# Kernel optimization log

Hardware: AMD Instinct MI355X
Metric: run time of the kernel (lower is better)

Reference implementation:

```python
import jax, jax.numpy as jnp
import numpy as np

T, B, I, H, O = 1024, 512, 32, 256, 32

def setup_inputs() -> dict:
    key = jax.random.key(0)
    ks = jax.random.split(key, 8)
    s_ih = 1.0 / np.sqrt(H)
    return {
        "input_states": jax.random.normal(ks[0], (T, B, I), jnp.float32),
        "physical_predictions": jax.random.normal(ks[1], (T, B, O), jnp.float32),
        "W_ih": jax.random.uniform(ks[2], (4 * H, I), jnp.float32, -s_ih, s_ih),
        "W_hh": jax.random.uniform(ks[3], (4 * H, H), jnp.float32, -s_ih, s_ih),
        "b_ih": jax.random.uniform(ks[4], (4 * H,), jnp.float32, -s_ih, s_ih),
        "b_hh": jax.random.uniform(ks[5], (4 * H,), jnp.float32, -s_ih, s_ih),
        "W_out": jax.random.uniform(ks[6], (O, H), jnp.float32, -s_ih, s_ih),
        "b_out": jax.random.uniform(ks[7], (O,), jnp.float32, -s_ih, s_ih),
    }

def reference(input_states, physical_predictions, W_ih, W_hh, b_ih, b_hh, W_out, b_out):
    # Teacher-forced LSTM rollout (teacher_force_probability=0 -> always use input_sequence[t]),
    # use_physics_as_bias=1 -> full_pred = physical_predictions[t] + linear(h_t).
    Bsz = input_states.shape[1]
    Hd = W_hh.shape[1]
    dt = input_states.dtype

    def step(carry, xs):
        h, c = carry
        x, phys = xs                                   # [B,I], [B,O]
        gates = x @ W_ih.T + b_ih + h @ W_hh.T + b_hh  # [B,4H]
        i_g, f_g, g_g, o_g = jnp.split(gates, 4, axis=-1)
        i_g = jax.nn.sigmoid(i_g)
        f_g = jax.nn.sigmoid(f_g)
        g_g = jnp.tanh(g_g)
        o_g = jax.nn.sigmoid(o_g)
        c = f_g * c + i_g * g_g
        h = o_g * jnp.tanh(c)
        rnn_pred = h @ W_out.T + b_out                 # [B,O]
        full_pred = phys + rnn_pred
        return (h, c), (full_pred, rnn_pred)

    h0 = jnp.zeros((Bsz, Hd), dt)
    c0 = jnp.zeros((Bsz, Hd), dt)
    _, (full_preds, rnn_preds) = jax.lax.scan(step, (h0, c0), (input_states, physical_predictions))
    # torch.stack(preds, 1) -> [B, T, O]
    return jnp.transpose(full_preds, (1, 0, 2)), jnp.transpose(rnn_preds, (1, 0, 2))
```

## Files before the change

kernel.cpp:

```cpp
#include <hip/hip_runtime.h>
#include <hip/hip_bf16.h>
#include <stdint.h>

typedef unsigned short u16;
typedef unsigned long long u64;
typedef __attribute__((ext_vector_type(8))) _Float16 f16x8;
typedef __attribute__((ext_vector_type(4))) float f32x4;

#define TSTEPS 1024
#define BATCH  512
#define INDIM  32
#define HID    256
#define ODIM   32
#define NCH    66
#define KCH    9

#define WS_BC   (NCH*KCH*64*8*2)
#define WS_XBUF (WS_BC + 4096)

#define MFMA(a,b,c) __builtin_amdgcn_mfma_f32_16x16x32_f16((a),(b),(c),0,0,0)
#define AGL(p)   __hip_atomic_load((p),      __ATOMIC_RELAXED, __HIP_MEMORY_SCOPE_AGENT)
#define AGS(p,v) __hip_atomic_store((p),(v), __ATOMIC_RELAXED, __HIP_MEMORY_SCOPE_AGENT)

__device__ __forceinline__ u16 f2h(float v){ _Float16 h=(_Float16)v; return *(u16*)&h; }
__device__ __forceinline__ float sigf(float x){ return 1.0f/(1.0f+__expf(-x)); }
__device__ __forceinline__ float tanhf_(float x){
    float ax=fabsf(x); float e=__expf(-2.f*ax); float t=(1.f-e)/(1.f+e); return copysignf(t,x);
}
__device__ __forceinline__ f16x8 frag_from_u64(u64 lo, u64 hi){
    union { u64 q[2]; f16x8 v; } u; u.q[0]=lo; u.q[1]=hi; return u.v;
}
__device__ __forceinline__ f16x8 cvt8(float4 a, float4 b){
    f16x8 r;
    r[0]=(_Float16)a.x; r[1]=(_Float16)a.y; r[2]=(_Float16)a.z; r[3]=(_Float16)a.w;
    r[4]=(_Float16)b.x; r[5]=(_Float16)b.y; r[6]=(_Float16)b.z; r[7]=(_Float16)b.w;
    return r;
}

__global__ __launch_bounds__(256) void prepack_kernel(
    const float* __restrict__ W_ih, const float* __restrict__ W_hh,
    const float* __restrict__ b_ih, const float* __restrict__ b_hh,
    const float* __restrict__ W_out,
    u16* __restrict__ Wb, float* __restrict__ Bc)
{
    int tid = blockIdx.x*blockDim.x + threadIdx.x;
    int stride = gridDim.x*blockDim.x;
    const int TOT = NCH*KCH*64*8;
    for (int idx = tid; idx < TOT; idx += stride) {
        int j    = idx & 7;
        int lane = (idx >> 3) & 63;
        int ck   = idx >> 9;
        int kc   = ck % KCH;
        int c    = ck / KCH;
        int kl   = ((lane >> 4) << 3) + j;
        float v;
        if (c < 64) {
            int g = c >> 4;
            int m = (c & 15) * 16 + (lane & 15);
            if (kc < 8) v = W_hh[(g*HID + m)*HID + (kc*32 + kl)];
            else        v = W_ih[(g*HID + m)*INDIM + kl];
        } else {
            int o = ((c - 64) << 4) + (lane & 15);
            v = (kc < 8) ? W_out[o*HID + kc*32 + kl] : 0.f;
        }
        Wb[idx] = f2h(v);
    }
    for (int n = tid; n < 1024; n += stride) {
        int c = n >> 4, qq = n & 15;
        int g = c >> 4;
        int m = (c & 15) * 16 + qq;
        Bc[n] = b_ih[g*HID + m] + b_hh[g*HID + m];
    }
}

__global__ __launch_bounds__(256) void init_xbuf_kernel(u64* __restrict__ xb) {
    int i = blockIdx.x*256 + threadIdx.x;
    AGS(xb + i, 1ull);
}

__global__ __launch_bounds__(64, 1) void lstm_kernel(
    const float* __restrict__ xin,
    const float* __restrict__ phys,
    const u16*  __restrict__ Wb_,
    const float* __restrict__ Bc,
    const float* __restrict__ b_out,
    u64* __restrict__ xb,
    float* __restrict__ out)
{
    const int lane = threadIdx.x;
    const int bid  = blockIdx.x;
    const int tile = bid >> 4;
    const int ug   = bid & 15;
    const int b0   = tile << 4;
    const int q    = lane & 15;
    const int rg   = lane >> 4;
    const int mrb  = rg << 2;

    __shared__ u16 scr[256];

    const f16x8* Wb8 = (const f16x8*)Wb_;

    f16x8 wg0[KCH], wg1[KCH], wg2[KCH], wg3[KCH];
#pragma unroll
    for (int kc = 0; kc < KCH; ++kc) {
        wg0[kc] = Wb8[((0*16+ug)*KCH + kc)*64 + lane];
        wg1[kc] = Wb8[((1*16+ug)*KCH + kc)*64 + lane];
        wg2[kc] = Wb8[((2*16+ug)*KCH + kc)*64 + lane];
        wg3[kc] = Wb8[((3*16+ug)*KCH + kc)*64 + lane];
    }
    f16x8 wp[8];
#pragma unroll
    for (int kc = 0; kc < 8; ++kc)
        wp[kc] = Wb8[((64 + (ug>>3))*KCH + kc)*64 + lane];

    const float bi0 = Bc[((0*16+ug)<<4)+q];
    const float bi1 = Bc[((1*16+ug)<<4)+q];
    const float bi2 = Bc[((2*16+ug)<<4)+q];
    const float bi3 = Bc[((3*16+ug)<<4)+q];

    const bool  isP = (ug == 0) || (ug == 8);
    const int   o_  = ((ug >> 3) << 4) + q;
    const float bip = isP ? b_out[o_] : 0.f;

    float ph0=0.f, ph1=0.f, ph2=0.f, ph3=0.f;
    if (isP) {
        ph0 = phys[(size_t)(b0+mrb+0)*ODIM + o_];
        ph1 = phys[(size_t)(b0+mrb+1)*ODIM + o_];
        ph2 = phys[(size_t)(b0+mrb+2)*ODIM + o_];
        ph3 = phys[(size_t)(b0+mrb+3)*ODIM + o_];
    }

    const float* xbase = xin + (size_t)(b0 + q)*INDIM + (rg << 3);
    float4 xc0 = *(const float4*)(xbase);
    float4 xc1 = *(const float4*)(xbase + 4);
    float4 xn0 = *(const float4*)(xbase + (size_t)BATCH*INDIM);
    float4 xn1 = *(const float4*)(xbase + (size_t)BATCH*INDIM + 4);

    const int m_ = (lane>>1) & 15, s_ = lane>>5, c_ = lane & 1;
    const int gw = ((m_ + 16*(((ug&1)<<1) + s_)) << 1) + c_;
    const int kcSelf = ug >> 1;
    u64* xbT = xb + (size_t)tile*2048;

    float* outFull = out;
    float* outRnn  = out + (size_t)BATCH*TSTEPS*ODIM;

    float cs0=0.f, cs1=0.f, cs2=0.f, cs3=0.f;
    f16x8 h0,h1,h2,h3,h4,h5,h6,h7;

    for (int t = 0; t < TSTEPS; ++t) {
        if (t > 0) {
            const u64* src = xbT + (size_t)(t&1)*1024 + lane*2;
            const u64 gexp = (u64)(((t-1) >> 1) & 1);
            u64 v0,v1,v2,v3,v4,v5,v6,v7,v8,v9,v10,v11,v12,v13,v14,v15;
            for (;;) {
                v0 =AGL(src+0*128); v1 =AGL(src+0*128+1);
                v2 =AGL(src+1*128); v3 =AGL(src+1*128+1);
                v4 =AGL(src+2*128); v5 =AGL(src+2*128+1);
                v6 =AGL(src+3*128); v7 =AGL(src+3*128+1);
                v8 =AGL(src+4*128); v9 =AGL(src+4*128+1);
                v10=AGL(src+5*128); v11=AGL(src+5*128+1);
                v12=AGL(src+6*128); v13=AGL(src+6*128+1);
                v14=AGL(src+7*128); v15=AGL(src+7*128+1);
                u64 bad = ((v0^gexp)|(v1^gexp)|(v2^gexp)|(v3^gexp)
                          |(v4^gexp)|(v5^gexp)|(v6^gexp)|(v7^gexp)
                          |(v8^gexp)|(v9^gexp)|(v10^gexp)|(v11^gexp)
                          |(v12^gexp)|(v13^gexp)|(v14^gexp)|(v15^gexp)) & 1ull;
                if (!__any((int)bad)) break;
            }
            h0=frag_from_u64(v0,v1);   h1=frag_from_u64(v2,v3);
            h2=frag_from_u64(v4,v5);   h3=frag_from_u64(v6,v7);
            h4=frag_from_u64(v8,v9);   h5=frag_from_u64(v10,v11);
            h6=frag_from_u64(v12,v13); h7=frag_from_u64(v14,v15);
        }

        f32x4 a0={bi0,bi0,bi0,bi0}, a1={bi1,bi1,bi1,bi1};
        f32x4 a2={bi2,bi2,bi2,bi2}, a3={bi3,bi3,bi3,bi3};
        {
            f16x8 ax = cvt8(xc0, xc1);
            a0=MFMA(ax,wg0[8],a0); a1=MFMA(ax,wg1[8],a1);
            a2=MFMA(ax,wg2[8],a2); a3=MFMA(ax,wg3[8],a3);
        }
        if (t > 0) {
            a0=MFMA(h0,wg0[0],a0); a1=MFMA(h0,wg1[0],a1); a2=MFMA(h0,wg2[0],a2); a3=MFMA(h0,wg3[0],a3);
            a0=MFMA(h1,wg0[1],a0); a1=MFMA(h1,wg1[1],a1); a2=MFMA(h1,wg2[1],a2); a3=MFMA(h1,wg3[1],a3);
            a0=MFMA(h2,wg0[2],a0); a1=MFMA(h2,wg1[2],a1); a2=MFMA(h2,wg2[2],a2); a3=MFMA(h2,wg3[2],a3);
            a0=MFMA(h3,wg0[3],a0); a1=MFMA(h3,wg1[3],a1); a2=MFMA(h3,wg2[3],a2); a3=MFMA(h3,wg3[3],a3);
            a0=MFMA(h4,wg0[4],a0); a1=MFMA(h4,wg1[4],a1); a2=MFMA(h4,wg2[4],a2); a3=MFMA(h4,wg3[4],a3);
            a0=MFMA(h5,wg0[5],a0); a1=MFMA(h5,wg1[5],a1); a2=MFMA(h5,wg2[5],a2); a3=MFMA(h5,wg3[5],a3);
            a0=MFMA(h6,wg0[6],a0); a1=MFMA(h6,wg1[6],a1); a2=MFMA(h6,wg2[6],a2); a3=MFMA(h6,wg3[6],a3);
            a0=MFMA(h7,wg0[7],a0); a1=MFMA(h7,wg1[7],a1); a2=MFMA(h7,wg2[7],a2); a3=MFMA(h7,wg3[7],a3);
        }

        {
            int tt = (t+2 < TSTEPS) ? (t+2) : (TSTEPS-1);
            const float* p = xbase + (size_t)tt*BATCH*INDIM;
            float4 nn0 = *(const float4*)p;
            float4 nn1 = *(const float4*)(p + 4);
            xc0 = xn0; xc1 = xn1; xn0 = nn0; xn1 = nn1;
        }

        if (isP && t > 0) {
            f32x4 pa = {bip,bip,bip,bip};
            pa=MFMA(h0,wp[0],pa); pa=MFMA(h1,wp[1],pa);
            pa=MFMA(h2,wp[2],pa); pa=MFMA(h3,wp[3],pa);
            pa=MFMA(h4,wp[4],pa); pa=MFMA(h5,wp[5],pa);
            pa=MFMA(h6,wp[6],pa); pa=MFMA(h7,wp[7],pa);
            const size_t ob = (size_t)(b0+mrb)*TSTEPS*ODIM + (size_t)(t-1)*ODIM + o_;
            const size_t rs = (size_t)TSTEPS*ODIM;
            outFull[ob+0*rs] = ph0 + pa[0];  outRnn[ob+0*rs] = pa[0];
            outFull[ob+1*rs] = ph1 + pa[1];  outRnn[ob+1*rs] = pa[1];
            outFull[ob+2*rs] = ph2 + pa[2];  outRnn[ob+2*rs] = pa[2];
            outFull[ob+3*rs] = ph3 + pa[3];  outRnn[ob+3*rs] = pa[3];
            const float* pb = phys + (size_t)t*BATCH*ODIM + (size_t)(b0+mrb)*ODIM + o_;
            ph0 = pb[0*ODIM]; ph1 = pb[1*ODIM]; ph2 = pb[2*ODIM]; ph3 = pb[3*ODIM];
        }

        {
            float gi,gf,gg,go,hv;
            gi=sigf(a0[0]); gf=sigf(a1[0]); gg=tanhf_(a2[0]); go=sigf(a3[0]);
            cs0 = gf*cs0 + gi*gg; hv = go*tanhf_(cs0);
            scr[(mrb+0 + 16*(q>>3))*8 + (q&7)] = f2h(hv);
            gi=sigf(a0[1]); gf=sigf(a1[1]); gg=tanhf_(a2[1]); go=sigf(a3[1]);
            cs1 = gf*cs1 + gi*gg; hv = go*tanhf_(cs1);
            scr[(mrb+1 + 16*(q>>3))*8 + (q&7)] = f2h(hv);
            gi=sigf(a0[2]); gf=sigf(a1[2]); gg=tanhf_(a2[2]); go=sigf(a3[2]);
            cs2 = gf*cs2 + gi*gg; hv = go*tanhf_(cs2);
            scr[(mrb+2 + 16*(q>>3))*8 + (q&7)] = f2h(hv);
            gi=sigf(a0[3]); gf=sigf(a1[3]); gg=tanhf_(a2[3]); go=sigf(a3[3]);
            cs3 = gf*cs3 + gi*gg; hv = go*tanhf_(cs3);
            scr[(mrb+3 + 16*(q>>3))*8 + (q&7)] = f2h(hv);

            u16 w0b=scr[lane*4+0], w1b=scr[lane*4+1], w2b=scr[lane*4+2], w3b=scr[lane*4+3];
            u64 pub = (u64)w0b | ((u64)w1b<<16) | ((u64)w2b<<32) | ((u64)w3b<<48);
            pub = (pub & ~1ull) | (u64)((t>>1)&1);
            AGS(xbT + (size_t)((t+1)&1)*1024 + kcSelf*128 + gw, pub);
        }
    }

    if (isP) {
        const u64* src = xbT + lane*2;
        u64 v0,v1,v2,v3,v4,v5,v6,v7,v8,v9,v10,v11,v12,v13,v14,v15;
        for (;;) {
            v0 =AGL(src+0*128); v1 =AGL(src+0*128+1);
            v2 =AGL(src+1*128); v3 =AGL(src+1*128+1);
            v4 =AGL(src+2*128); v5 =AGL(src+2*128+1);
            v6 =AGL(src+3*128); v7 =AGL(src+3*128+1);
            v8 =AGL(src+4*128); v9 =AGL(src+4*128+1);
            v10=AGL(src+5*128); v11=AGL(src+5*128+1);
            v12=AGL(src+6*128); v13=AGL(src+6*128+1);
            v14=AGL(src+7*128); v15=AGL(src+7*128+1);
            u64 bad = ((v0^1ull)|(v1^1ull)|(v2^1ull)|(v3^1ull)
                      |(v4^1ull)|(v5^1ull)|(v6^1ull)|(v7^1ull)
                      |(v8^1ull)|(v9^1ull)|(v10^1ull)|(v11^1ull)
                      |(v12^1ull)|(v13^1ull)|(v14^1ull)|(v15^1ull)) & 1ull;
            if (!__any((int)bad)) break;
        }
        h0=frag_from_u64(v0,v1);   h1=frag_from_u64(v2,v3);
        h2=frag_from_u64(v4,v5);   h3=frag_from_u64(v6,v7);
        h4=frag_from_u64(v8,v9);   h5=frag_from_u64(v10,v11);
        h6=frag_from_u64(v12,v13); h7=frag_from_u64(v14,v15);

        f32x4 pa = {bip,bip,bip,bip};
        pa=MFMA(h0,wp[0],pa); pa=MFMA(h1,wp[1],pa);
        pa=MFMA(h2,wp[2],pa); pa=MFMA(h3,wp[3],pa);
        pa=MFMA(h4,wp[4],pa); pa=MFMA(h5,wp[5],pa);
        pa=MFMA(h6,wp[6],pa); pa=MFMA(h7,wp[7],pa);
        const size_t ob = (size_t)(b0+mrb)*TSTEPS*ODIM + (size_t)1023*ODIM + o_;
        const size_t rs = (size_t)TSTEPS*ODIM;
        outFull[ob+0*rs] = ph0 + pa[0];  outRnn[ob+0*rs] = pa[0];
        outFull[ob+1*rs] = ph1 + pa[1];  outRnn[ob+1*rs] = pa[1];
        outFull[ob+2*rs] = ph2 + pa[2];  outRnn[ob+2*rs] = pa[2];
        outFull[ob+3*rs] = ph3 + pa[3];  outRnn[ob+3*rs] = pa[3];
    }
}

extern "C" void kernel_launch(void* const* d_in, const int* in_sizes, int n_in,
                              void* d_out, int out_size, void* d_ws, size_t ws_size,
                              hipStream_t stream) {
    const float* xin   = (const float*)d_in[0];
    const float* phys  = (const float*)d_in[1];
    const float* W_ih  = (const float*)d_in[2];
    const float* W_hh  = (const float*)d_in[3];
    const float* b_ih  = (const float*)d_in[4];
    const float* b_hh  = (const float*)d_in[5];
    const float* W_out = (const float*)d_in[6];
    const float* b_out = (const float*)d_in[7];

    char*  ws = (char*)d_ws;
    u16*   Wb = (u16*)ws;
    float* Bc = (float*)(ws + WS_BC);
    u64*   xb = (u64*)(ws + WS_XBUF);

    prepack_kernel<<<256, 256, 0, stream>>>(W_ih, W_hh, b_ih, b_hh, W_out, Wb, Bc);
    init_xbuf_kernel<<<256, 256, 0, stream>>>(xb);
    lstm_kernel<<<512, 64, 0, stream>>>(xin, phys, Wb, Bc, b_out, xb, (float*)d_out);
}
```

Before: 2.729 ms.

## Use sc0 vectorized loads for h exchange with atomic fallback and reorder work

Each step's exchange of hidden-state fragments between workgroups now polls with wide dwordx4 loads carrying the sc0 cache bit, in place of sixteen relaxed 64-bit atomic loads. Every publish writes both a sc0-stored copy and an atomic-stored copy. If fast polling spins 256 times without seeing the expected parity, the wave falls back to the atomic copy. The block-to-tile mapping is interleaved, and the output projection and x prefetch move after the publish so the critical path shortens. The risk is memory-model subtlety: sc0 loads may not see cross-CU writes promptly, and every store is now doubled.

```diff
diff --git a/kernel.cpp b/kernel.cpp
--- a/kernel.cpp
+++ b/kernel.cpp
@@ -3,6 +3,8 @@
 #include <stdint.h>
 
 typedef unsigned short u16;
+typedef unsigned char  u8;
+typedef unsigned int   u32;
 typedef unsigned long long u64;
 typedef __attribute__((ext_vector_type(8))) _Float16 f16x8;
 typedef __attribute__((ext_vector_type(4))) float f32x4;
@@ -15,8 +17,9 @@
 #define NCH    66
 #define KCH    9
 
-#define WS_BC   (NCH*KCH*64*8*2)
-#define WS_XBUF (WS_BC + 4096)
+#define WS_BC (NCH*KCH*64*8*2)
+#define WS_XP (WS_BC + 4096)
+#define WS_XS (WS_XP + 32*2*8*128*8)
 
 #define MFMA(a,b,c) __builtin_amdgcn_mfma_f32_16x16x32_f16((a),(b),(c),0,0,0)
 #define AGL(p)   __hip_atomic_load((p),      __ATOMIC_RELAXED, __HIP_MEMORY_SCOPE_AGENT)
@@ -26,15 +29,27 @@
 __device__ __forceinline__ float sigf(float x){ return 1.0f/(1.0f+__expf(-x)); }
 __device__ __forceinline__ float tanhf_(float x){
     float ax=fabsf(x); float e=__expf(-2.f*ax); float t=(1.f-e)/(1.f+e); return copysignf(t,x);
-}
-__device__ __forceinline__ f16x8 frag_from_u64(u64 lo, u64 hi){
-    union { u64 q[2]; f16x8 v; } u; u.q[0]=lo; u.q[1]=hi; return u.v;
 }
 __device__ __forceinline__ f16x8 cvt8(float4 a, float4 b){
     f16x8 r;
     r[0]=(_Float16)a.x; r[1]=(_Float16)a.y; r[2]=(_Float16)a.z; r[3]=(_Float16)a.w;
     r[4]=(_Float16)b.x; r[5]=(_Float16)b.y; r[6]=(_Float16)b.z; r[7]=(_Float16)b.w;
     return r;
+}
+
+__device__ __forceinline__ void ld4_sc0(const u8* p, uint4& a, uint4& b, uint4& c, uint4& d){
+    asm volatile(
+        "global_load_dwordx4 %0, %4, off sc0\n\t"
+        "global_load_dwordx4 %1, %4, off offset:1024 sc0\n\t"
+        "global_load_dwordx4 %2, %4, off offset:2048 sc0\n\t"
+        "global_load_dwordx4 %3, %4, off offset:3072 sc0\n\t"
+        "s_waitcnt vmcnt(0)"
+        : "=&v"(a), "=&v"(b), "=&v"(c), "=&v"(d)
+        : "v"(p) : "memory");
+    __builtin_amdgcn_sched_barrier(0);
+}
+__device__ __forceinline__ void st_u64_sc0(u64* p, u64 v){
+    asm volatile("global_store_dwordx2 %0, %1, off sc0" :: "v"(p), "v"(v) : "memory");
 }
 
 __global__ __launch_bounds__(256) void prepack_kernel(
@@ -73,9 +88,10 @@
     }
 }
 
-__global__ __launch_bounds__(256) void init_xbuf_kernel(u64* __restrict__ xb) {
+__global__ __launch_bounds__(256) void init_xbuf_kernel(u64* __restrict__ xp, u64* __restrict__ xs) {
     int i = blockIdx.x*256 + threadIdx.x;
-    AGS(xb + i, 1ull);
+    AGS(xp + i, 1ull);
+    AGS(xs + i, 1ull);
 }
 
 __global__ __launch_bounds__(64, 1) void lstm_kernel(
@@ -84,13 +100,14 @@
     const u16*  __restrict__ Wb_,
     const float* __restrict__ Bc,
     const float* __restrict__ b_out,
-    u64* __restrict__ xb,
+    u64* __restrict__ xp,
+    u64* __restrict__ xs,
     float* __restrict__ out)
 {
     const int lane = threadIdx.x;
     const int bid  = blockIdx.x;
-    const int tile = bid >> 4;
-    const int ug   = bid & 15;
+    const int tile = bid & 31;
+    const int ug   = bid >> 5;
     const int b0   = tile << 4;
     const int q    = lane & 15;
     const int rg   = lane >> 4;
@@ -139,40 +156,17 @@
     const int m_ = (lane>>1) & 15, s_ = lane>>5, c_ = lane & 1;
     const int gw = ((m_ + 16*(((ug&1)<<1) + s_)) << 1) + c_;
     const int kcSelf = ug >> 1;
-    u64* xbT = xb + (size_t)tile*2048;
+    u64* xpT = xp + (size_t)tile*2048;
+    u64* xsT = xs + (size_t)tile*2048;
 
     float* outFull = out;
     float* outRnn  = out + (size_t)BATCH*TSTEPS*ODIM;
 
     float cs0=0.f, cs1=0.f, cs2=0.f, cs3=0.f;
     f16x8 h0,h1,h2,h3,h4,h5,h6,h7;
+    bool fastm = true;
 
     for (int t = 0; t < TSTEPS; ++t) {
-        if (t > 0) {
-            const u64* src = xbT + (size_t)(t&1)*1024 + lane*2;
-            const u64 gexp = (u64)(((t-1) >> 1) & 1);
-            u64 v0,v1,v2,v3,v4,v5,v6,v7,v8,v9,v10,v11,v12,v13,v14,v15;
-            for (;;) {
-                v0 =AGL(src+0*128); v1 =AGL(src+0*128+1);
-                v2 =AGL(src+1*128); v3 =AGL(src+1*128+1);
-                v4 =AGL(src+2*128); v5 =AGL(src+2*128+1);
-                v6 =AGL(src+3*128); v7 =AGL(src+3*128+1);
-                v8 =AGL(src+4*128); v9 =AGL(src+4*128+1);
-                v10=AGL(src+5*128); v11=AGL(src+5*128+1);
-                v12=AGL(src+6*128); v13=AGL(src+6*128+1);
-                v14=AGL(src+7*128); v15=AGL(src+7*128+1);
-                u64 bad = ((v0^gexp)|(v1^gexp)|(v2^gexp)|(v3^gexp)
-                          |(v4^gexp)|(v5^gexp)|(v6^gexp)|(v7^gexp)
-                          |(v8^gexp)|(v9^gexp)|(v10^gexp)|(v11^gexp)
-                          |(v12^gexp)|(v13^gexp)|(v14^gexp)|(v15^gexp)) & 1ull;
-                if (!__any((int)bad)) break;
-            }
-            h0=frag_from_u64(v0,v1);   h1=frag_from_u64(v2,v3);
-            h2=frag_from_u64(v4,v5);   h3=frag_from_u64(v6,v7);
-            h4=frag_from_u64(v8,v9);   h5=frag_from_u64(v10,v11);
-            h6=frag_from_u64(v12,v13); h7=frag_from_u64(v14,v15);
-        }
-
         f32x4 a0={bi0,bi0,bi0,bi0}, a1={bi1,bi1,bi1,bi1};
         f32x4 a2={bi2,bi2,bi2,bi2}, a3={bi3,bi3,bi3,bi3};
         {
@@ -180,7 +174,35 @@
             a0=MFMA(ax,wg0[8],a0); a1=MFMA(ax,wg1[8],a1);
             a2=MFMA(ax,wg2[8],a2); a3=MFMA(ax,wg3[8],a3);
         }
+
         if (t > 0) {
+            const u8*  pb = (const u8*)xpT + (size_t)(t&1)*8192 + lane*16;
+            const u64* sb = xsT + (size_t)(t&1)*1024 + lane*2;
+            const u32  gx = (u32)(((t-1) >> 1) & 1);
+            union U { uint4 u; f16x8 h; u64 qq[2]; } A,B,C,D,E,F,G,H;
+            int iter = 0;
+            for (;;) {
+                if (fastm) {
+                    ld4_sc0(pb,        A.u,B.u,C.u,D.u);
+                    ld4_sc0(pb + 4096, E.u,F.u,G.u,H.u);
+                } else {
+                    A.qq[0]=AGL(sb+0*128); A.qq[1]=AGL(sb+0*128+1);
+                    B.qq[0]=AGL(sb+1*128); B.qq[1]=AGL(sb+1*128+1);
+                    C.qq[0]=AGL(sb+2*128); C.qq[1]=AGL(sb+2*128+1);
+                    D.qq[0]=AGL(sb+3*128); D.qq[1]=AGL(sb+3*128+1);
+                    E.qq[0]=AGL(sb+4*128); E.qq[1]=AGL(sb+4*128+1);
+                    F.qq[0]=AGL(sb+5*128); F.qq[1]=AGL(sb+5*128+1);
+                    G.qq[0]=AGL(sb+6*128); G.qq[1]=AGL(sb+6*128+1);
+                    H.qq[0]=AGL(sb+7*128); H.qq[1]=AGL(sb+7*128+1);
+                }
+                u32 bad = ((A.u.x^gx)|(A.u.z^gx)|(B.u.x^gx)|(B.u.z^gx)
+                          |(C.u.x^gx)|(C.u.z^gx)|(D.u.x^gx)|(D.u.z^gx)
+                          |(E.u.x^gx)|(E.u.z^gx)|(F.u.x^gx)|(F.u.z^gx)
+                          |(G.u.x^gx)|(G.u.z^gx)|(H.u.x^gx)|(H.u.z^gx)) & 1u;
+                if (!__any((int)bad)) { h0=A.h;h1=B.h;h2=C.h;h3=D.h;h4=E.h;h5=F.h;h6=G.h;h7=H.h; break; }
+                if (fastm && ++iter >= 256) fastm = false;
+            }
+
             a0=MFMA(h0,wg0[0],a0); a1=MFMA(h0,wg1[0],a1); a2=MFMA(h0,wg2[0],a2); a3=MFMA(h0,wg3[0],a3);
             a0=MFMA(h1,wg0[1],a0); a1=MFMA(h1,wg1[1],a1); a2=MFMA(h1,wg2[1],a2); a3=MFMA(h1,wg3[1],a3);
             a0=MFMA(h2,wg0[2],a0); a1=MFMA(h2,wg1[2],a1); a2=MFMA(h2,wg2[2],a2); a3=MFMA(h2,wg3[2],a3);
@@ -189,30 +211,6 @@
             a0=MFMA(h5,wg0[5],a0); a1=MFMA(h5,wg1[5],a1); a2=MFMA(h5,wg2[5],a2); a3=MFMA(h5,wg3[5],a3);
             a0=MFMA(h6,wg0[6],a0); a1=MFMA(h6,wg1[6],a1); a2=MFMA(h6,wg2[6],a2); a3=MFMA(h6,wg3[6],a3);
             a0=MFMA(h7,wg0[7],a0); a1=MFMA(h7,wg1[7],a1); a2=MFMA(h7,wg2[7],a2); a3=MFMA(h7,wg3[7],a3);
-        }
-
-        {
-            int tt = (t+2 < TSTEPS) ? (t+2) : (TSTEPS-1);
-            const float* p = xbase + (size_t)tt*BATCH*INDIM;
-            float4 nn0 = *(const float4*)p;
-            float4 nn1 = *(const float4*)(p + 4);
-            xc0 = xn0; xc1 = xn1; xn0 = nn0; xn1 = nn1;
-        }
-
-        if (isP && t > 0) {
-            f32x4 pa = {bip,bip,bip,bip};
-            pa=MFMA(h0,wp[0],pa); pa=MFMA(h1,wp[1],pa);
-            pa=MFMA(h2,wp[2],pa); pa=MFMA(h3,wp[3],pa);
-            pa=MFMA(h4,wp[4],pa); pa=MFMA(h5,wp[5],pa);
-            pa=MFMA(h6,wp[6],pa); pa=MFMA(h7,wp[7],pa);
-            const size_t ob = (size_t)(b0+mrb)*TSTEPS*ODIM + (size_t)(t-1)*ODIM + o_;
-            const size_t rs = (size_t)TSTEPS*ODIM;
-            outFull[ob+0*rs] = ph0 + pa[0];  outRnn[ob+0*rs] = pa[0];
-            outFull[ob+1*rs] = ph1 + pa[1];  outRnn[ob+1*rs] = pa[1];
-            outFull[ob+2*rs] = ph2 + pa[2];  outRnn[ob+2*rs] = pa[2];
-            outFull[ob+3*rs] = ph3 + pa[3];  outRnn[ob+3*rs] = pa[3];
-            const float* pb = phys + (size_t)t*BATCH*ODIM + (size_t)(b0+mrb)*ODIM + o_;
-            ph0 = pb[0*ODIM]; ph1 = pb[1*ODIM]; ph2 = pb[2*ODIM]; ph3 = pb[3*ODIM];
         }
 
         {
@@ -233,33 +231,62 @@
             u16 w0b=scr[lane*4+0], w1b=scr[lane*4+1], w2b=scr[lane*4+2], w3b=scr[lane*4+3];
             u64 pub = (u64)w0b | ((u64)w1b<<16) | ((u64)w2b<<32) | ((u64)w3b<<48);
             pub = (pub & ~1ull) | (u64)((t>>1)&1);
-            AGS(xbT + (size_t)((t+1)&1)*1024 + kcSelf*128 + gw, pub);
+            const size_t off = (size_t)((t+1)&1)*1024 + kcSelf*128 + gw;
+            st_u64_sc0(xpT + off, pub);
+            AGS(xsT + off, pub);
+        }
+
+        if (isP && t > 0) {
+            f32x4 pa = {bip,bip,bip,bip};
+            pa=MFMA(h0,wp[0],pa); pa=MFMA(h1,wp[1],pa);
+            pa=MFMA(h2,wp[2],pa); pa=MFMA(h3,wp[3],pa);
+            pa=MFMA(h4,wp[4],pa); pa=MFMA(h5,wp[5],pa);
+            pa=MFMA(h6,wp[6],pa); pa=MFMA(h7,wp[7],pa);
+            const size_t ob = (size_t)(b0+mrb)*TSTEPS*ODIM + (size_t)(t-1)*ODIM + o_;
+            const size_t rs = (size_t)TSTEPS*ODIM;
+            outFull[ob+0*rs] = ph0 + pa[0];  outRnn[ob+0*rs] = pa[0];
+            outFull[ob+1*rs] = ph1 + pa[1];  outRnn[ob+1*rs] = pa[1];
+            outFull[ob+2*rs] = ph2 + pa[2];  outRnn[ob+2*rs] = pa[2];
+            outFull[ob+3*rs] = ph3 + pa[3];  outRnn[ob+3*rs] = pa[3];
+            const float* pb2 = phys + (size_t)t*BATCH*ODIM + (size_t)(b0+mrb)*ODIM + o_;
+            ph0 = pb2[0*ODIM]; ph1 = pb2[1*ODIM]; ph2 = pb2[2*ODIM]; ph3 = pb2[3*ODIM];
+        }
+
+        {
+            int tt = (t+2 < TSTEPS) ? (t+2) : (TSTEPS-1);
+            const float* p = xbase + (size_t)tt*BATCH*INDIM;
+            float4 nn0 = *(const float4*)p;
+            float4 nn1 = *(const float4*)(p + 4);
+            xc0 = xn0; xc1 = xn1; xn0 = nn0; xn1 = nn1;
         }
     }
 
     if (isP) {
-        const u64* src = xbT + lane*2;
-        u64 v0,v1,v2,v3,v4,v5,v6,v7,v8,v9,v10,v11,v12,v13,v14,v15;
+        const u8*  pb = (const u8*)xpT + lane*16;
+        const u64* sb = xsT + lane*2;
+        union U { uint4 u; f16x8 h; u64 qq[2]; } A,B,C,D,E,F,G,H;
+        int iter = 0;
         for (;;) {
-            v0 =AGL(src+0*128); v1 =AGL(src+0*128+1);
-            v2 =AGL(src+1*128); v3 =AGL(src+1*128+1);
-            v4 =AGL(src+2*128); v5 =AGL(src+2*128+1);
-            v6 =AGL(src+3*128); v7 =AGL(src+3*128+1);
-            v8 =AGL(src+4*128); v9 =AGL(src+4*128+1);
-            v10=AGL(src+5*128); v11=AGL(src+5*128+1);
-            v12=AGL(src+6*128); v13=AGL(src+6*128+1);
-            v14=AGL(src+7*128); v15=AGL(src+7*128+1);
-            u64 bad = ((v0^1ull)|(v1^1ull)|(v2^1ull)|(v3^1ull)
-                      |(v4^1ull)|(v5^1ull)|(v6^1ull)|(v7^1ull)
-                      |(v8^1ull)|(v9^1ull)|(v10^1ull)|(v11^1ull)
-                      |(v12^1ull)|(v13^1ull)|(v14^1ull)|(v15^1ull)) & 1ull;
-            if (!__any((int)bad)) break;
-        }
-        h0=frag_from_u64(v0,v1);   h1=frag_from_u64(v2,v3);
-        h2=frag_from_u64(v4,v5);   h3=frag_from_u64(v6,v7);
-        h4=frag_from_u64(v8,v9);   h5=frag_from_u64(v10,v11);
-        h6=frag_from_u64(v12,v13); h7=frag_from_u64(v14,v15);
-
+            if (fastm) {
+                ld4_sc0(pb,        A.u,B.u,C.u,D.u);
+                ld4_sc0(pb + 4096, E.u,F.u,G.u,H.u);
+            } else {
+                A.qq[0]=AGL(sb+0*128); A.qq[1]=AGL(sb+0*128+1);
+                B.qq[0]=AGL(sb+1*128); B.qq[1]=AGL(sb+1*128+1);
+                C.qq[0]=AGL(sb+2*128); C.qq[1]=AGL(sb+2*128+1);
+                D.qq[0]=AGL(sb+3*128); D.qq[1]=AGL(sb+3*128+1);
+                E.qq[0]=AGL(sb+4*128); E.qq[1]=AGL(sb+4*128+1);
+                F.qq[0]=AGL(sb+5*128); F.qq[1]=AGL(sb+5*128+1);
+                G.qq[0]=AGL(sb+6*128); G.qq[1]=AGL(sb+6*128+1);
+                H.qq[0]=AGL(sb+7*128); H.qq[1]=AGL(sb+7*128+1);
+            }
+            u32 bad = ((A.u.x^1u)|(A.u.z^1u)|(B.u.x^1u)|(B.u.z^1u)
+                      |(C.u.x^1u)|(C.u.z^1u)|(D.u.x^1u)|(D.u.z^1u)
+                      |(E.u.x^1u)|(E.u.z^1u)|(F.u.x^1u)|(F.u.z^1u)
+                      |(G.u.x^1u)|(G.u.z^1u)|(H.u.x^1u)|(H.u.z^1u)) & 1u;
+            if (!__any((int)bad)) { h0=A.h;h1=B.h;h2=C.h;h3=D.h;h4=E.h;h5=F.h;h6=G.h;h7=H.h; break; }
+            if (fastm && ++iter >= 256) fastm = false;
+        }
         f32x4 pa = {bip,bip,bip,bip};
         pa=MFMA(h0,wp[0],pa); pa=MFMA(h1,wp[1],pa);
         pa=MFMA(h2,wp[2],pa); pa=MFMA(h3,wp[3],pa);
@@ -289,9 +316,10 @@
     char*  ws = (char*)d_ws;
     u16*   Wb = (u16*)ws;
     float* Bc = (float*)(ws + WS_BC);
-    u64*   xb = (u64*)(ws + WS_XBUF);
+    u64*   xp = (u64*)(ws + WS_XP);
+    u64*   xs = (u64*)(ws + WS_XS);
 
     prepack_kernel<<<256, 256, 0, stream>>>(W_ih, W_hh, b_ih, b_hh, W_out, Wb, Bc);
-    init_xbuf_kernel<<<256, 256, 0, stream>>>(xb);
-    lstm_kernel<<<512, 64, 0, stream>>>(xin, phys, Wb, Bc, b_out, xb, (float*)d_out);
-}
+    init_xbuf_kernel<<<256, 256, 0, stream>>>(xp, xs);
+    lstm_kernel<<<512, 64, 0, stream>>>(xin, phys, Wb, Bc, b_out, xp, xs, (float*)d_out);
+}
```

Result: faster. 2.214 ms (-18.9%).
